# Optimization experiments

Hardware: AMD Instinct MI355X
Metric: run time of the kernel (lower is better)

## Reference

```python
import jax, jax.numpy as jnp
import numpy as np

L, B, S, D, H = 6, 2, 2048, 512, 8
DH = D // H
FF = 4 * D
EPS = 1e-5


def setup_inputs() -> dict:
    key = jax.random.key(0)
    ks = jax.random.split(key, 10)
    w = lambda k, shape: jax.random.normal(k, shape, jnp.float32) * 0.02
    return {
        "query": jax.random.normal(ks[0], (B, S, D), jnp.float32),
        "key": jax.random.normal(ks[1], (B, S, D), jnp.float32),
        "query_mask": jnp.ones((B, S), jnp.int32),
        "key_mask": jnp.ones((B, S), jnp.int32),
        # per-layer stacked params; conv1d(kernel=1) == linear with weight [out,in]
        "Wq": w(ks[2], (L, D, D)), "bq": jnp.zeros((L, D), jnp.float32),
        "Wk": w(ks[3], (L, D, D)), "bk": jnp.zeros((L, D), jnp.float32),
        "Wv": w(ks[4], (L, D, D)), "bv": jnp.zeros((L, D), jnp.float32),
        "Wo": w(ks[5], (L, D, D)), "bo": jnp.zeros((L, D), jnp.float32),
        "ln1_g": jnp.ones((L, D), jnp.float32), "ln1_b": jnp.zeros((L, D), jnp.float32),
        "ff_w1": w(ks[6], (L, FF, D)), "ff_b1": jnp.zeros((L, FF), jnp.float32),
        "ff_w2": w(ks[7], (L, D, FF)), "ff_b2": jnp.zeros((L, D), jnp.float32),
        "ln2_g": jnp.ones((L, D), jnp.float32), "ln2_b": jnp.zeros((L, D), jnp.float32),
    }


def _layer_norm(x, g, b):
    m = jnp.mean(x, axis=-1, keepdims=True)
    v = jnp.mean(jnp.square(x - m), axis=-1, keepdims=True)
    return (x - m) * jax.lax.rsqrt(v + EPS) * g + b


def reference(query, key, query_mask, key_mask,
              Wq, bq, Wk, bk, Wv, bv, Wo, bo,
              ln1_g, ln1_b, ff_w1, ff_b1, ff_w2, ff_b2, ln2_g, ln2_b):
    b_, s_, d_ = query.shape
    kpad = (key_mask == 0)[:, None, None, :]          # [B,1,1,K]
    qm = query_mask.astype(query.dtype)[:, :, None]    # [B,S,1]
    x = query
    for i in range(L):
        # QKV projections (conv1d kernel-size-1 == linear), split heads -> [B,H,S,DH]
        def split(t):
            return t.reshape(b_, s_, H, DH).transpose(0, 2, 1, 3)
        q = split(x @ Wq[i].T + bq[i]) * (float(DH) ** -0.5)
        k = split(key @ Wk[i].T + bk[i])
        v = split(key @ Wv[i].T + bv[i])
        attn = jnp.einsum('bhqd,bhkd->bhqk', q, k)
        attn = jnp.where(kpad, -jnp.inf, attn)
        attn = jax.nn.softmax(attn, axis=-1)
        o = jnp.einsum('bhqk,bhkd->bhqd', attn, v)
        o = o.transpose(0, 2, 1, 3).reshape(b_, s_, H * DH)
        o = (o @ Wo[i].T + bo[i]) * qm                 # output proj + query mask
        x = _layer_norm(o + x, ln1_g[i], ln1_b[i])
        h = jax.nn.leaky_relu(x @ ff_w1[i].T + ff_b1[i], 0.01)
        f = (h @ ff_w2[i].T + ff_b2[i]) * qm           # FFN mask on output
        x = _layer_norm(f + x, ln2_g[i], ln2_b[i])
    return x
```

## Files before the change

### kernel.cpp

```cpp
#include <hip/hip_runtime.h>
#include <stdint.h>

constexpr int LAYERS = 6;
constexpr int Bc = 2, Sc = 2048, Dc = 512, Hc = 8, DHc = 64, FFc = 2048;
constexpr int Mc = Bc * Sc;
constexpr int NS = 2;
constexpr int KCHUNK = Sc / NS;

typedef __attribute__((ext_vector_type(8))) __bf16 bf16x8;
typedef __attribute__((ext_vector_type(4))) __bf16 bf16x4;
typedef __attribute__((ext_vector_type(4))) float f32x4;

__device__ __forceinline__ void async_ld16(const void* g, void* lds) {
  __builtin_amdgcn_global_load_lds(
      (const __attribute__((address_space(1))) uint32_t*)g,
      (__attribute__((address_space(3))) uint32_t*)lds, 16, 0, 0);
}

__global__ __launch_bounds__(256) void cvt_kernel(const float* __restrict__ in,
                                                  __bf16* __restrict__ out, int n) {
  int i = (blockIdx.x * 256 + threadIdx.x) * 4;
  if (i + 4 > n) return;
  const float4 v = *(const float4*)(in + i);
  bf16x4 o;
  o[0] = (__bf16)v.x; o[1] = (__bf16)v.y; o[2] = (__bf16)v.z; o[3] = (__bf16)v.w;
  *(bf16x4*)(out + i) = o;
}

__global__ __launch_bounds__(256) void cvt_kv_kernel(const float* __restrict__ Wk,
                                                     const float* __restrict__ Wv,
                                                     __bf16* __restrict__ out) {
  size_t i = ((size_t)blockIdx.x * 256 + threadIdx.x) * 4;
  int n = (int)(i / ((size_t)Dc * Dc));
  int lyr = n >> 1, p = n & 1;
  size_t idx = i - (size_t)n * Dc * Dc;
  const float* src = (p ? Wv : Wk) + (size_t)lyr * Dc * Dc + idx;
  const float4 v = *(const float4*)src;
  bf16x4 o;
  o[0] = (__bf16)v.x; o[1] = (__bf16)v.y; o[2] = (__bf16)v.z; o[3] = (__bf16)v.w;
  *(bf16x4*)(out + i) = o;
}

__global__ __launch_bounds__(256) void kbias_kernel(const int* __restrict__ km,
                                                    float* __restrict__ kb, int n) {
  int i = blockIdx.x * 256 + threadIdx.x;
  if (i < n) kb[i] = km[i] ? 0.f : -1e30f;
}

template <int BM, int BN, int WM, int WN, int EPI>
__global__ __launch_bounds__(256) void gemm_bt(
    const __bf16* __restrict__ A, const __bf16* __restrict__ W,
    const float* __restrict__ bias, const float* __restrict__ bias2,
    float* __restrict__ outf, __bf16* __restrict__ outb,
    __bf16* __restrict__ outb2, float scale,
    int M, int N, int K, int Kstride) {
  constexpr int BK = 64;
  __shared__ __bf16 As[2][BM * BK];
  __shared__ __bf16 Bs[2][BN * BK];
  const int tid = threadIdx.x;
  const int l15 = tid & 15;
  const int lg = (tid & 63) >> 4;
  const int w = tid >> 6;
  const int wm = w >> 1, wn = w & 1;
  const int tm = blockIdx.y * BM;
  const int tn = blockIdx.x * BN;
  const int z = blockIdx.z;
  const __bf16* Ap = A + (size_t)tm * Kstride + (size_t)z * K;
  const __bf16* Wp = W + (size_t)tn * Kstride + (size_t)z * K;
  f32x4 acc[WM][WN] = {};

  auto stage = [&](int k0, int bf) {
#pragma unroll
    for (int c = 0; c < BM * 8 / 256; ++c) {
      int cc = c * 256 + tid;
      int r = cc >> 3, s = cc & 7;
      int ss = s ^ (r & 7);
      async_ld16(Ap + (size_t)r * Kstride + k0 + ss * 8, &As[bf][cc * 8]);
    }
#pragma unroll
    for (int c = 0; c < BN * 8 / 256; ++c) {
      int cc = c * 256 + tid;
      int r = cc >> 3, s = cc & 7;
      int ss = s ^ (r & 7);
      async_ld16(Wp + (size_t)r * Kstride + k0 + ss * 8, &Bs[bf][cc * 8]);
    }
  };

  const int nk = K / BK;
  stage(0, 0);
  __syncthreads();
  int buf = 0;
  for (int t = 0; t < nk; ++t) {
    if (t + 1 < nk) stage((t + 1) * BK, buf ^ 1);
    bf16x8 af[WM][2], bfr[WN][2];
#pragma unroll
    for (int i = 0; i < WM; ++i) {
      int row = wm * WM * 16 + i * 16 + l15;
#pragma unroll
      for (int kf = 0; kf < 2; ++kf)
        af[i][kf] = *(const bf16x8*)&As[buf][row * 64 + (((kf * 4 + lg) ^ (row & 7)) * 8)];
    }
#pragma unroll
    for (int j = 0; j < WN; ++j) {
      int row = wn * WN * 16 + j * 16 + l15;
#pragma unroll
      for (int kf = 0; kf < 2; ++kf)
        bfr[j][kf] = *(const bf16x8*)&Bs[buf][row * 64 + (((kf * 4 + lg) ^ (row & 7)) * 8)];
    }
#pragma unroll
    for (int kf = 0; kf < 2; ++kf)
#pragma unroll
      for (int i = 0; i < WM; ++i)
#pragma unroll
        for (int j = 0; j < WN; ++j)
          acc[i][j] = __builtin_amdgcn_mfma_f32_16x16x32_bf16(af[i][kf], bfr[j][kf], acc[i][j], 0, 0, 0);
    __syncthreads();
    buf ^= 1;
  }

#pragma unroll
  for (int i = 0; i < WM; ++i) {
#pragma unroll
    for (int j = 0; j < WN; ++j) {
      const int n = tn + wn * WN * 16 + j * 16 + l15;
      float bv;
      if constexpr (EPI == 6) {
        int lyr = n >> 10, w1 = n & 1023, p = w1 >> 9, d = w1 & 511;
        bv = (p ? bias2 : bias)[lyr * 512 + d];
      } else if constexpr (EPI == 0) {
        bv = (z == 0) ? bias[n] : 0.f;
      } else {
        bv = bias[n];
      }
#pragma unroll
      for (int r = 0; r < 4; ++r) {
        const int m = tm + wm * WM * 16 + i * 16 + lg * 4 + r;
        float v = acc[i][j][r] + bv;
        if constexpr (EPI == 0) {
          outf[(size_t)z * M * N + (size_t)m * N + n] = v;
        } else if constexpr (EPI == 1) {
          int b = m >> 11, s = m & (Sc - 1);
          int h = n >> 6, dh = n & 63;
          outb[(((size_t)(b * Hc + h)) * Sc + s) * DHc + dh] = (__bf16)(v * scale);
        } else if constexpr (EPI == 4) {
          float lv = v > 0.f ? v : 0.01f * v;
          outb[(size_t)m * N + n] = (__bf16)lv;
        } else if constexpr (EPI == 6) {
          int b = m >> 11, s = m & (Sc - 1);
          int lyr = n >> 10, w1 = n & 1023, p = w1 >> 9, d = w1 & 511;
          int h = d >> 6, dh = d & 63;
          if (p == 0)
            outb[((((size_t)(lyr * Bc + b) * Hc + h)) * Sc + s) * DHc + dh] = (__bf16)v;
          else
            outb2[((((size_t)(lyr * Bc + b) * Hc + h)) * DHc + dh) * Sc + s] = (__bf16)v;
        }
      }
    }
  }
}

__global__ __launch_bounds__(256, 4) void attn_kernel(
    const __bf16* __restrict__ q, const __bf16* __restrict__ k,
    const __bf16* __restrict__ vt, const float* __restrict__ kb,
    __bf16* __restrict__ Opart, float* __restrict__ mpart,
    float* __restrict__ lpart) {
  const int bh = blockIdx.y;
  const int b = bh >> 3;
  const int z = blockIdx.z;
  const int w = threadIdx.x >> 6;
  const int l = threadIdx.x & 63;
  const int l15 = l & 15;
  const int lg = l >> 4;
  const int tid = threadIdx.x;
  const int qbase = blockIdx.x * 64 + w * 16;
  const int k0 = z * KCHUNK;

  const __bf16* qp = q + ((size_t)bh * Sc + qbase) * DHc;
  const __bf16* kp = k + (size_t)bh * Sc * DHc;
  const __bf16* vp = vt + (size_t)bh * DHc * Sc;
  const float* kbp = kb + (size_t)b * Sc;

  bf16x8 qf[2];
  qf[0] = *(const bf16x8*)(qp + l15 * DHc + lg * 8);
  qf[1] = *(const bf16x8*)(qp + l15 * DHc + 32 + lg * 8);

  bf16x8 onesf;
#pragma unroll
  for (int i = 0; i < 8; ++i) onesf[i] = (__bf16)1.0f;

  f32x4 oacc[4] = {};
  f32x4 lacc = {};
  float mr[4] = {-1e30f, -1e30f, -1e30f, -1e30f};

  __shared__ __bf16 Ks[2][4096];
  __shared__ __bf16 Vs[2][4096];
  __shared__ __bf16 P[4][1024];

  auto stage = [&](int t, int bf) {
    const int kt = k0 + t * 64;
#pragma unroll
    for (int ii = 0; ii < 2; ++ii) {
      int i = ii * 256 + tid;
      int r = i >> 3;
      int bsrc = (i & 7) ^ (r & 7);
      async_ld16(kp + (size_t)(kt + r) * DHc + bsrc * 8, &Ks[bf][i * 8]);
      async_ld16(vp + (size_t)r * Sc + kt + bsrc * 8, &Vs[bf][i * 8]);
    }
  };

  float mb[4];
#pragma unroll
  for (int cb = 0; cb < 4; ++cb) mb[cb] = kbp[k0 + cb * 16 + l15];
  stage(0, 0);
  __syncthreads();

  constexpr int NT = KCHUNK / 64;
  int buf = 0;
  for (int t = 0; t < NT; ++t) {
    const int kt = k0 + t * 64;
    if (t + 1 < NT) stage(t + 1, buf ^ 1);
    float mbn[4];
    if (t + 1 < NT) {
#pragma unroll
      for (int cb = 0; cb < 4; ++cb) mbn[cb] = kbp[kt + 64 + cb * 16 + l15];
    }

    f32x4 sacc[4] = {};
#pragma unroll
    for (int kf = 0; kf < 2; ++kf) {
#pragma unroll
      for (int cb = 0; cb < 4; ++cb) {
        int row = cb * 16 + l15;
        bf16x8 kfr = *(const bf16x8*)&Ks[buf][row * 64 + (((kf * 4 + lg) ^ (row & 7)) * 8)];
        sacc[cb] = __builtin_amdgcn_mfma_f32_16x16x32_bf16(qf[kf], kfr, sacc[cb], 0, 0, 0);
      }
    }
#pragma unroll
    for (int cb = 0; cb < 4; ++cb) {
#pragma unroll
      for (int j = 0; j < 4; ++j) sacc[cb][j] += mb[cb];
    }
    float mx[4];
#pragma unroll
    for (int j = 0; j < 4; ++j) {
      float m0 = fmaxf(fmaxf(sacc[0][j], sacc[1][j]), fmaxf(sacc[2][j], sacc[3][j]));
#pragma unroll
      for (int d = 1; d < 16; d <<= 1) m0 = fmaxf(m0, __shfl_xor(m0, d, 64));
      mx[j] = m0;
    }
    bool need = (mx[0] > mr[0] + 8.f) || (mx[1] > mr[1] + 8.f) ||
                (mx[2] > mr[2] + 8.f) || (mx[3] > mr[3] + 8.f);
    if (__any(need)) {
#pragma unroll
      for (int j = 0; j < 4; ++j) {
        float mn = fmaxf(mr[j], mx[j]);
        float f = __expf(mr[j] - mn);
        mr[j] = mn;
        lacc[j] *= f;
#pragma unroll
        for (int db = 0; db < 4; ++db) oacc[db][j] *= f;
      }
    }
#pragma unroll
    for (int cb = 0; cb < 4; ++cb)
#pragma unroll
      for (int j = 0; j < 4; ++j) sacc[cb][j] = __expf(sacc[cb][j] - mr[j]);

#pragma unroll
    for (int cb = 0; cb < 4; ++cb)
#pragma unroll
      for (int j = 0; j < 4; ++j) {
        int qrow = lg * 4 + j;
        P[w][qrow * 64 + ((cb * 16 + l15) ^ ((qrow & 7) << 3))] = (__bf16)sacc[cb][j];
      }
#pragma unroll
    for (int kf = 0; kf < 2; ++kf) {
      bf16x8 pf = *(const bf16x8*)&P[w][l15 * 64 + (((kf * 4 + lg) ^ (l15 & 7)) * 8)];
      lacc = __builtin_amdgcn_mfma_f32_16x16x32_bf16(pf, onesf, lacc, 0, 0, 0);
#pragma unroll
      for (int db = 0; db < 4; ++db) {
        int row = db * 16 + l15;
        bf16x8 vf = *(const bf16x8*)&Vs[buf][row * 64 + (((kf * 4 + lg) ^ (row & 7)) * 8)];
        oacc[db] = __builtin_amdgcn_mfma_f32_16x16x32_bf16(pf, vf, oacc[db], 0, 0, 0);
      }
    }
    if (t + 1 < NT) {
#pragma unroll
      for (int cb = 0; cb < 4; ++cb) mb[cb] = mbn[cb];
    }
    __syncthreads();
    buf ^= 1;
  }

  const size_t obase = (((size_t)(z * Bc * Hc + bh)) * Sc + qbase) * DHc;
#pragma unroll
  for (int db = 0; db < 4; ++db)
#pragma unroll
    for (int j = 0; j < 4; ++j)
      Opart[obase + (size_t)(lg * 4 + j) * DHc + db * 16 + l15] = (__bf16)oacc[db][j];
  if (l15 == 0) {
#pragma unroll
    for (int j = 0; j < 4; ++j) {
      int row = (z * Bc * Hc + bh) * Sc + qbase + lg * 4 + j;
      mpart[row] = mr[j];
      lpart[row] = lacc[j];
    }
  }
}

__global__ __launch_bounds__(256) void attn_combine(
    const __bf16* __restrict__ Opart, const float* __restrict__ mpart,
    const float* __restrict__ lpart, __bf16* __restrict__ out) {
  int t = blockIdx.x * 256 + threadIdx.x;
  int d = t & 63;
  int row = t >> 6;
  int bh = row >> 11, s = row & (Sc - 1);
  constexpr int RSTRIDE = Bc * Hc * Sc;
  float m0 = mpart[row], m1 = mpart[RSTRIDE + row];
  float l0 = lpart[row], l1 = lpart[RSTRIDE + row];
  float M = fmaxf(m0, m1);
  float e0 = __expf(m0 - M), e1 = __expf(m1 - M);
  float denom = e0 * l0 + e1 * l1;
  float o0 = (float)Opart[(size_t)row * DHc + d];
  float o1 = (float)Opart[((size_t)RSTRIDE + row) * DHc + d];
  float o = (e0 * o0 + e1 * o1) / denom;
  int b = bh >> 3, h = bh & 7;
  out[(((size_t)b * Sc + s)) * Dc + h * DHc + d] = (__bf16)o;
}

__global__ __launch_bounds__(256) void add_ln_kernel(
    const float* __restrict__ res, const float* __restrict__ res2,
    const int* __restrict__ rmask, const float* __restrict__ xin,
    const float* __restrict__ g, const float* __restrict__ bb,
    float* __restrict__ xo, __bf16* __restrict__ xbo) {
  const int row = blockIdx.x;
  const int tid = threadIdx.x;
  const float* rp = res + (size_t)row * Dc;
  const float* xp = xin + (size_t)row * Dc;
  float mfac = rmask ? (float)rmask[row] : 1.f;
  float a0 = rp[tid], a1 = rp[tid + 256];
  if (res2) {
    const float* r2p = res2 + (size_t)row * Dc;
    a0 += r2p[tid];
    a1 += r2p[tid + 256];
  }
  float v0 = a0 * mfac + xp[tid];
  float v1 = a1 * mfac + xp[tid + 256];
  float s = v0 + v1;
#pragma unroll
  for (int d = 1; d < 64; d <<= 1) s += __shfl_xor(s, d, 64);
  __shared__ float red[4], red2[4];
  if ((tid & 63) == 0) red[tid >> 6] = s;
  __syncthreads();
  float mean = (red[0] + red[1] + red[2] + red[3]) * (1.0f / Dc);
  float d0 = v0 - mean, d1 = v1 - mean;
  float qq = d0 * d0 + d1 * d1;
#pragma unroll
  for (int d = 1; d < 64; d <<= 1) qq += __shfl_xor(qq, d, 64);
  if ((tid & 63) == 0) red2[tid >> 6] = qq;
  __syncthreads();
  float var = (red2[0] + red2[1] + red2[2] + red2[3]) * (1.0f / Dc);
  float rs = rsqrtf(var + 1e-5f);
  float o0 = d0 * rs * g[tid] + bb[tid];
  float o1 = d1 * rs * g[tid + 256] + bb[tid + 256];
  xo[(size_t)row * Dc + tid] = o0;
  xo[(size_t)row * Dc + tid + 256] = o1;
  xbo[(size_t)row * Dc + tid] = (__bf16)o0;
  xbo[(size_t)row * Dc + tid + 256] = (__bf16)o1;
}

extern "C" void kernel_launch(void* const* d_in, const int* in_sizes, int n_in,
                              void* d_out, int out_size, void* d_ws, size_t ws_size,
                              hipStream_t stream) {
  (void)in_sizes; (void)n_in; (void)out_size; (void)ws_size;
  const float* query = (const float*)d_in[0];
  const float* key   = (const float*)d_in[1];
  const int* qmask   = (const int*)d_in[2];
  const int* kmask   = (const int*)d_in[3];
  const float* Wq = (const float*)d_in[4];
  const float* bq = (const float*)d_in[5];
  const float* Wk = (const float*)d_in[6];
  const float* bk = (const float*)d_in[7];
  const float* Wv = (const float*)d_in[8];
  const float* bv = (const float*)d_in[9];
  const float* Wo = (const float*)d_in[10];
  const float* bo = (const float*)d_in[11];
  const float* ln1g = (const float*)d_in[12];
  const float* ln1b = (const float*)d_in[13];
  const float* fw1 = (const float*)d_in[14];
  const float* fb1 = (const float*)d_in[15];
  const float* fw2 = (const float*)d_in[16];
  const float* fb2 = (const float*)d_in[17];
  const float* ln2g = (const float*)d_in[18];
  const float* ln2b = (const float*)d_in[19];

  char* ws = (char*)d_ws;
  size_t off = 0;
  auto carve = [&](size_t bytes) -> void* {
    void* p = ws + off;
    off += (bytes + 255) & ~(size_t)255;
    return p;
  };
  float* x_f    = (float*)carve((size_t)Mc * Dc * 4);
  float* tmp_f  = (float*)carve((size_t)2 * Mc * Dc * 4);
  __bf16* x_b   = (__bf16*)carve((size_t)Mc * Dc * 2);
  __bf16* key_b = (__bf16*)carve((size_t)Mc * Dc * 2);
  __bf16* q_b   = (__bf16*)carve((size_t)Mc * Dc * 2);
  __bf16* at_b  = (__bf16*)carve((size_t)Mc * Dc * 2);
  __bf16* h_b   = (__bf16*)carve((size_t)Mc * FFc * 2);
  __bf16* k_all = (__bf16*)carve((size_t)LAYERS * Mc * Dc * 2);
  __bf16* vt_all= (__bf16*)carve((size_t)LAYERS * Mc * Dc * 2);
  __bf16* wq_b  = (__bf16*)carve((size_t)LAYERS * Dc * Dc * 2);
  __bf16* wkv_b = (__bf16*)carve((size_t)LAYERS * 2 * Dc * Dc * 2);
  __bf16* wo_b  = (__bf16*)carve((size_t)LAYERS * Dc * Dc * 2);
  __bf16* w1_b  = (__bf16*)carve((size_t)LAYERS * FFc * Dc * 2);
  __bf16* w2_b  = (__bf16*)carve((size_t)LAYERS * Dc * FFc * 2);
  float* ml_f   = (float*)carve((size_t)NS * Bc * Hc * Sc * 4 * 2);
  float* kb_f   = (float*)carve((size_t)Bc * Sc * 4);

  __bf16* opart_b = h_b;
  float* mpart_f = ml_f;
  float* lpart_f = ml_f + (size_t)NS * Bc * Hc * Sc;
  float* tmp2_f = tmp_f + (size_t)Mc * Dc;

  auto cvt = [&](const float* src, __bf16* dst, int n) {
    cvt_kernel<<<n / 1024, 256, 0, stream>>>(src, dst, n);
  };
  cvt(query, x_b, Mc * Dc);
  cvt(key, key_b, Mc * Dc);
  cvt(Wq, wq_b, LAYERS * Dc * Dc);
  cvt_kv_kernel<<<LAYERS * 2 * Dc * Dc / 1024, 256, 0, stream>>>(Wk, Wv, wkv_b);
  cvt(Wo, wo_b, LAYERS * Dc * Dc);
  cvt(fw1, w1_b, LAYERS * FFc * Dc);
  cvt(fw2, w2_b, LAYERS * Dc * FFc);
  kbias_kernel<<<Bc * Sc / 256, 256, 0, stream>>>(kmask, kb_f, Bc * Sc);
  hipMemcpyAsync(x_f, query, (size_t)Mc * Dc * 4, hipMemcpyDeviceToDevice, stream);

  const dim3 blk(256);
  const dim3 gP64(Dc / 64, Mc / 64);
  const dim3 gOP(Dc / 64, Mc / 64, 2);
  const dim3 gFF2(Dc / 64, Mc / 64, 2);
  const dim3 gKV(LAYERS * 2 * Dc / 128, Mc / 64);
  const dim3 gFF1(FFc / 128, Mc / 64);
  const dim3 gAttn(Sc / 64, Bc * Hc, NS);
  const dim3 gComb(Bc * Hc * Sc * DHc / 256);

  gemm_bt<64, 128, 2, 4, 6><<<gKV, blk, 0, stream>>>(
      key_b, wkv_b, bk, bv, nullptr, k_all, vt_all, 1.0f,
      Mc, LAYERS * 2 * Dc, Dc, Dc);

  for (int i = 0; i < LAYERS; ++i) {
    const __bf16* wq_i = wq_b + (size_t)i * Dc * Dc;
    const __bf16* wo_i = wo_b + (size_t)i * Dc * Dc;
    const __bf16* w1_i = w1_b + (size_t)i * FFc * Dc;
    const __bf16* w2_i = w2_b + (size_t)i * Dc * FFc;
    const __bf16* k_i  = k_all + (size_t)i * Mc * Dc;
    const __bf16* vt_i = vt_all + (size_t)i * Mc * Dc;

    gemm_bt<64, 64, 2, 2, 1><<<gP64, blk, 0, stream>>>(
        x_b, wq_i, bq + i * Dc, nullptr, nullptr, q_b, nullptr, 0.125f,
        Mc, Dc, Dc, Dc);
    attn_kernel<<<gAttn, blk, 0, stream>>>(q_b, k_i, vt_i, kb_f,
                                           opart_b, mpart_f, lpart_f);
    attn_combine<<<gComb, blk, 0, stream>>>(opart_b, mpart_f, lpart_f, at_b);
    gemm_bt<64, 64, 2, 2, 0><<<gOP, blk, 0, stream>>>(
        at_b, wo_i, bo + i * Dc, nullptr, tmp_f, nullptr, nullptr, 1.0f,
        Mc, Dc, Dc / 2, Dc);
    add_ln_kernel<<<Mc, blk, 0, stream>>>(tmp_f, tmp2_f, qmask, x_f,
                                          ln1g + i * Dc, ln1b + i * Dc, x_f, x_b);
    gemm_bt<64, 128, 2, 4, 4><<<gFF1, blk, 0, stream>>>(
        x_b, w1_i, fb1 + i * FFc, nullptr, nullptr, h_b, nullptr, 1.0f,
        Mc, FFc, Dc, Dc);
    gemm_bt<64, 64, 2, 2, 0><<<gFF2, blk, 0, stream>>>(
        h_b, w2_i, fb2 + i * Dc, nullptr, tmp_f, nullptr, nullptr, 1.0f,
        Mc, Dc, FFc / 2, FFc);
    add_ln_kernel<<<Mc, blk, 0, stream>>>(tmp_f, tmp2_f, qmask, x_f,
                                          ln2g + i * Dc, ln2b + i * Dc, x_f, x_b);
  }
  hipMemcpyAsync(d_out, x_f, (size_t)Mc * Dc * 4, hipMemcpyDeviceToDevice, stream);
}
```

Baseline: 876.1 us.

## Transpose V via LDS in KV epilogue, load V directly in attention, retile FF1

The KV projection epilogue now stages V tiles in shared memory so it can write the transposed V layout with coalesced 16-byte stores, replacing scattered 2-byte stores. The attention kernel drops the V shared-memory double buffer and loads V fragments from global memory into registers, which cuts LDS use and lets the launch bound request 5 blocks per SM. Key-bias loads are no longer prefetched one tile ahead. The FF1 GEMM moves to 64x64 tiles, doubling the number of blocks. Direct global V loads could add latency inside the attention loop, and the smaller FF1 tiles get less data reuse per block.

```diff
diff --git a/kernel.cpp b/kernel.cpp
--- a/kernel.cpp
+++ b/kernel.cpp
@@ -118,16 +118,69 @@
     buf ^= 1;
   }
 
+  if constexpr (EPI == 6) {
+    const bool isV = ((tn & 1023) >= 512);
+    const int lyr = tn >> 10;
+    const int b = tm >> 11;
+    const int sbase = tm & (Sc - 1);
+    if (isV) {
+      __bf16* T = (__bf16*)&As[0][0];
+#pragma unroll
+      for (int i = 0; i < WM; ++i) {
+#pragma unroll
+        for (int j = 0; j < WN; ++j) {
+          const int d = wn * WN * 16 + j * 16 + l15;
+          const int dg = (tn & 511) + d;
+          const float bv = bias2[lyr * 512 + dg];
+          const int s0 = wm * WM * 16 + i * 16 + lg * 4;
+          bf16x4 pk;
+#pragma unroll
+          for (int r = 0; r < 4; ++r) pk[r] = (__bf16)(acc[i][j][r] + bv);
+          const int slot = (s0 >> 3) ^ (d & 7);
+          *(bf16x4*)&T[d * 64 + slot * 8 + (s0 & 7)] = pk;
+        }
+      }
+      __syncthreads();
+      const int rr = tid >> 3;
+      const int c8 = tid & 7;
+#pragma unroll
+      for (int pass = 0; pass < 4; ++pass) {
+        const int d = pass * 32 + rr;
+        const int slot = c8 ^ (d & 7);
+        bf16x8 v8 = *(const bf16x8*)&T[d * 64 + slot * 8];
+        const int dg = (tn & 511) + d;
+        const int h = dg >> 6, dh = dg & 63;
+        *(bf16x8*)&outb2[((((size_t)(lyr * Bc + b) * Hc + h)) * DHc + dh) * Sc +
+                         sbase + c8 * 8] = v8;
+      }
+    } else {
+#pragma unroll
+      for (int i = 0; i < WM; ++i) {
+#pragma unroll
+        for (int j = 0; j < WN; ++j) {
+          const int d = wn * WN * 16 + j * 16 + l15;
+          const int dg = (tn & 511) + d;
+          const float bv = bias[lyr * 512 + dg];
+          const int h = dg >> 6, dh = dg & 63;
+#pragma unroll
+          for (int r = 0; r < 4; ++r) {
+            const int s = sbase + wm * WM * 16 + i * 16 + lg * 4 + r;
+            outb[((((size_t)(lyr * Bc + b) * Hc + h)) * Sc + s) * DHc + dh] =
+                (__bf16)(acc[i][j][r] + bv);
+          }
+        }
+      }
+    }
+    return;
+  }
+
 #pragma unroll
   for (int i = 0; i < WM; ++i) {
 #pragma unroll
     for (int j = 0; j < WN; ++j) {
       const int n = tn + wn * WN * 16 + j * 16 + l15;
       float bv;
-      if constexpr (EPI == 6) {
-        int lyr = n >> 10, w1 = n & 1023, p = w1 >> 9, d = w1 & 511;
-        bv = (p ? bias2 : bias)[lyr * 512 + d];
-      } else if constexpr (EPI == 0) {
+      if constexpr (EPI == 0) {
         bv = (z == 0) ? bias[n] : 0.f;
       } else {
         bv = bias[n];
@@ -145,21 +198,13 @@
         } else if constexpr (EPI == 4) {
           float lv = v > 0.f ? v : 0.01f * v;
           outb[(size_t)m * N + n] = (__bf16)lv;
-        } else if constexpr (EPI == 6) {
-          int b = m >> 11, s = m & (Sc - 1);
-          int lyr = n >> 10, w1 = n & 1023, p = w1 >> 9, d = w1 & 511;
-          int h = d >> 6, dh = d & 63;
-          if (p == 0)
-            outb[((((size_t)(lyr * Bc + b) * Hc + h)) * Sc + s) * DHc + dh] = (__bf16)v;
-          else
-            outb2[((((size_t)(lyr * Bc + b) * Hc + h)) * DHc + dh) * Sc + s] = (__bf16)v;
         }
       }
     }
   }
 }
 
-__global__ __launch_bounds__(256, 4) void attn_kernel(
+__global__ __launch_bounds__(256, 5) void attn_kernel(
     const __bf16* __restrict__ q, const __bf16* __restrict__ k,
     const __bf16* __restrict__ vt, const float* __restrict__ kb,
     __bf16* __restrict__ Opart, float* __restrict__ mpart,
@@ -193,10 +238,9 @@
   float mr[4] = {-1e30f, -1e30f, -1e30f, -1e30f};
 
   __shared__ __bf16 Ks[2][4096];
-  __shared__ __bf16 Vs[2][4096];
   __shared__ __bf16 P[4][1024];
 
-  auto stage = [&](int t, int bf) {
+  auto stageK = [&](int t, int bf) {
     const int kt = k0 + t * 64;
 #pragma unroll
     for (int ii = 0; ii < 2; ++ii) {
@@ -204,26 +248,25 @@
       int r = i >> 3;
       int bsrc = (i & 7) ^ (r & 7);
       async_ld16(kp + (size_t)(kt + r) * DHc + bsrc * 8, &Ks[bf][i * 8]);
-      async_ld16(vp + (size_t)r * Sc + kt + bsrc * 8, &Vs[bf][i * 8]);
     }
   };
 
-  float mb[4];
-#pragma unroll
-  for (int cb = 0; cb < 4; ++cb) mb[cb] = kbp[k0 + cb * 16 + l15];
-  stage(0, 0);
+  stageK(0, 0);
   __syncthreads();
 
   constexpr int NT = KCHUNK / 64;
   int buf = 0;
   for (int t = 0; t < NT; ++t) {
     const int kt = k0 + t * 64;
-    if (t + 1 < NT) stage(t + 1, buf ^ 1);
-    float mbn[4];
-    if (t + 1 < NT) {
-#pragma unroll
-      for (int cb = 0; cb < 4; ++cb) mbn[cb] = kbp[kt + 64 + cb * 16 + l15];
-    }
+    if (t + 1 < NT) stageK(t + 1, buf ^ 1);
+
+    float mb[4];
+#pragma unroll
+    for (int cb = 0; cb < 4; ++cb) mb[cb] = kbp[kt + cb * 16 + l15];
+    bf16x8 vf0[4];
+#pragma unroll
+    for (int db = 0; db < 4; ++db)
+      vf0[db] = *(const bf16x8*)(vp + (size_t)(db * 16 + l15) * Sc + kt + lg * 8);
 
     f32x4 sacc[4] = {};
 #pragma unroll
@@ -273,20 +316,24 @@
         int qrow = lg * 4 + j;
         P[w][qrow * 64 + ((cb * 16 + l15) ^ ((qrow & 7) << 3))] = (__bf16)sacc[cb][j];
       }
-#pragma unroll
-    for (int kf = 0; kf < 2; ++kf) {
-      bf16x8 pf = *(const bf16x8*)&P[w][l15 * 64 + (((kf * 4 + lg) ^ (l15 & 7)) * 8)];
+    bf16x8 vf1[4];
+#pragma unroll
+    for (int db = 0; db < 4; ++db)
+      vf1[db] = *(const bf16x8*)(vp + (size_t)(db * 16 + l15) * Sc + kt + 32 + lg * 8);
+
+    {
+      bf16x8 pf = *(const bf16x8*)&P[w][l15 * 64 + ((lg ^ (l15 & 7)) * 8)];
       lacc = __builtin_amdgcn_mfma_f32_16x16x32_bf16(pf, onesf, lacc, 0, 0, 0);
 #pragma unroll
-      for (int db = 0; db < 4; ++db) {
-        int row = db * 16 + l15;
-        bf16x8 vf = *(const bf16x8*)&Vs[buf][row * 64 + (((kf * 4 + lg) ^ (row & 7)) * 8)];
-        oacc[db] = __builtin_amdgcn_mfma_f32_16x16x32_bf16(pf, vf, oacc[db], 0, 0, 0);
-      }
-    }
-    if (t + 1 < NT) {
-#pragma unroll
-      for (int cb = 0; cb < 4; ++cb) mb[cb] = mbn[cb];
+      for (int db = 0; db < 4; ++db)
+        oacc[db] = __builtin_amdgcn_mfma_f32_16x16x32_bf16(pf, vf0[db], oacc[db], 0, 0, 0);
+    }
+    {
+      bf16x8 pf = *(const bf16x8*)&P[w][l15 * 64 + ((((4 + lg)) ^ (l15 & 7)) * 8)];
+      lacc = __builtin_amdgcn_mfma_f32_16x16x32_bf16(pf, onesf, lacc, 0, 0, 0);
+#pragma unroll
+      for (int db = 0; db < 4; ++db)
+        oacc[db] = __builtin_amdgcn_mfma_f32_16x16x32_bf16(pf, vf1[db], oacc[db], 0, 0, 0);
     }
     __syncthreads();
     buf ^= 1;
@@ -441,7 +488,7 @@
   const dim3 gOP(Dc / 64, Mc / 64, 2);
   const dim3 gFF2(Dc / 64, Mc / 64, 2);
   const dim3 gKV(LAYERS * 2 * Dc / 128, Mc / 64);
-  const dim3 gFF1(FFc / 128, Mc / 64);
+  const dim3 gFF1(FFc / 64, Mc / 64);
   const dim3 gAttn(Sc / 64, Bc * Hc, NS);
   const dim3 gComb(Bc * Hc * Sc * DHc / 256);
 
@@ -468,7 +515,7 @@
         Mc, Dc, Dc / 2, Dc);
     add_ln_kernel<<<Mc, blk, 0, stream>>>(tmp_f, tmp2_f, qmask, x_f,
                                           ln1g + i * Dc, ln1b + i * Dc, x_f, x_b);
-    gemm_bt<64, 128, 2, 4, 4><<<gFF1, blk, 0, stream>>>(
+    gemm_bt<64, 64, 2, 2, 4><<<gFF1, blk, 0, stream>>>(
         x_b, w1_i, fb1 + i * FFc, nullptr, nullptr, h_b, nullptr, 1.0f,
         Mc, FFc, Dc, Dc);
     gemm_bt<64, 64, 2, 2, 0><<<gFF2, blk, 0, stream>>>(
```

Result: slower. 1.625 ms (+85.5%).
